# Performance work log

Measured on AMD Instinct MI355X. Metric: run time of the kernel, lower is better.

The kernel has to match this reference:

```python
import jax, jax.numpy as jnp
import numpy as np

N = 50000      # nodes
E = 600000     # edges
D = 128        # in_channels
H = 128        # hidden_channels
C = 16         # out_channels
L = 3          # num GIN layers
G = 512        # graphs in batch
BN_EPS = 1e-5


def setup_inputs() -> dict:
    key = jax.random.key(0)
    ks = jax.random.split(key, 18)
    s = 0.05
    x = jax.random.normal(ks[0], (N, D), jnp.float32)
    edge_index = jax.random.randint(ks[1], (2, E), 0, N, dtype=jnp.int32)
    batch = jnp.sort(jax.random.randint(ks[2], (N,), 0, G, dtype=jnp.int32))
    # per-layer GIN MLP params (in_channels == hidden, so layers stack uniformly)
    W1s = jax.random.normal(ks[3], (L, D, H), jnp.float32) * s
    b1s = jnp.zeros((L, H), jnp.float32)
    g1s = jnp.ones((L, H), jnp.float32)    # inner BatchNorm gamma
    be1s = jnp.zeros((L, H), jnp.float32)  # inner BatchNorm beta
    W2s = jax.random.normal(ks[4], (L, H, H), jnp.float32) * s
    b2s = jnp.zeros((L, H), jnp.float32)
    gns = jnp.ones((L, H), jnp.float32)    # outer (post-conv) BatchNorm gamma
    bns = jnp.zeros((L, H), jnp.float32)
    # classifier head
    Wc1 = jax.random.normal(ks[5], (H, H), jnp.float32) * s
    bc1 = jnp.zeros((H,), jnp.float32)
    gc = jnp.ones((H,), jnp.float32)
    bec = jnp.zeros((H,), jnp.float32)
    Wc2 = jax.random.normal(ks[6], (H, C), jnp.float32) * s
    bc2 = jnp.zeros((C,), jnp.float32)
    return dict(x=x, edge_index=edge_index, batch=batch, W1s=W1s, b1s=b1s,
                g1s=g1s, be1s=be1s, W2s=W2s, b2s=b2s, gns=gns, bns=bns,
                Wc1=Wc1, bc1=bc1, gc=gc, bec=bec, Wc2=Wc2, bc2=bc2)


def _bn(h, gamma, beta):
    # BatchNorm1d in training mode: batch statistics over the node/row dim
    m = jnp.mean(h, axis=0)
    v = jnp.mean((h - m) ** 2, axis=0)
    return gamma * (h - m) * jax.lax.rsqrt(v + BN_EPS) + beta


def reference(x, edge_index, batch, W1s, b1s, g1s, be1s, W2s, b2s, gns, bns,
              Wc1, bc1, gc, bec, Wc2, bc2):
    src, dst = edge_index[0], edge_index[1]
    h = x
    for l in range(L):
        # GINConv, eps=0: mlp((1+eps)*x_i + sum_{j->i} x_j)
        agg = jax.ops.segment_sum(h[src], dst, num_segments=N) + h
        z = agg @ W1s[l] + b1s[l]
        z = jax.nn.relu(_bn(z, g1s[l], be1s[l]))
        z = z @ W2s[l] + b2s[l]
        h = jax.nn.relu(_bn(z, gns[l], bns[l]))
    # global mean pool over graphs
    counts = jax.ops.segment_sum(jnp.ones((N,), h.dtype), batch, num_segments=G)
    pooled = jax.ops.segment_sum(h, batch, num_segments=G) / jnp.maximum(counts, 1.0)[:, None]
    z = pooled @ Wc1 + bc1
    z = jax.nn.relu(_bn(z, gc, bec))
    return z @ Wc2 + bc2  # [G, C]
```

## Files before the change

### kernel.cpp

```cpp
#include <hip/hip_runtime.h>
#include <hip/hip_fp16.h>

#define NN 50000
#define NE 600000
#define DIM 128
#define NG 512
#define OC 16
#define BN_EPS 1e-5f

typedef __attribute__((ext_vector_type(8))) short short8v;
typedef __attribute__((ext_vector_type(8))) _Float16 half8v;
typedef __attribute__((ext_vector_type(2))) _Float16 h2v;
typedef __attribute__((ext_vector_type(4))) float f32x4;

__device__ inline float hbits2f(short s) {
    __half_raw hr; hr.x = (unsigned short)s;
    return __half2float(__half(hr));
}
__device__ inline short f2hbits(float f) {
    __half h = __float2half(f);
    short r;
    __builtin_memcpy(&r, &h, 2);
    return r;
}
__device__ inline h2v u2p(unsigned u) {
    h2v h;
    __builtin_memcpy(&h, &u, 4);
    return h;
}
__device__ inline unsigned p2u(h2v h) {
    unsigned u;
    __builtin_memcpy(&u, &h, 4);
    return u;
}
__device__ inline h2v f2p(float a, float b) {
    h2v h;
    h[0] = (_Float16)a;
    h[1] = (_Float16)b;
    return h;
}

__global__ void k_setup(const float* __restrict__ W1s, const float* __restrict__ W2s,
                        const float* __restrict__ Wc1, unsigned short* __restrict__ wfrag,
                        const int* __restrict__ dstv, int* __restrict__ deg,
                        const float* __restrict__ x, __half* __restrict__ Ht) {
    int b = blockIdx.x;
    int t = threadIdx.x;
    if (b < 56) {
        int idx = b * 256 + t;
        int lane = idx & 63;
        int k0 = (idx >> 6) & 3;
        int ct = (idx >> 8) & 7;
        int m = idx >> 11;
        const float* Wsrc = (m < 3) ? (W1s + (size_t)m * 16384)
                          : (m < 6) ? (W2s + (size_t)(m - 3) * 16384)
                                    : Wc1;
        int colc = ct * 16 + (lane & 15);
        int kbase = k0 * 32 + (lane >> 4) * 8;
        short8v hi, lo;
#pragma unroll
        for (int j = 0; j < 8; j++) {
            float w = Wsrc[(size_t)(kbase + j) * 128 + colc];
            short hb = f2hbits(w);
            hi[j] = hb;
            lo[j] = f2hbits(w - hbits2f(hb));
        }
        size_t fo = ((size_t)(ct * 4 + k0) * 64 + lane) * 8;
        *(short8v*)(wfrag + (size_t)(m * 2 + 0) * 16384 + fo) = hi;
        *(short8v*)(wfrag + (size_t)(m * 2 + 1) * 16384 + fo) = lo;
    } else if (b < 2400) {
        int i = (b - 56) * 256 + t;
        if (i < NE) atomicAdd(&deg[dstv[i]], 1);
    } else {
        int i = (b - 2400) * 256 + t;
        float4 v = ((const float4*)x)[i];
        uint2 pk;
        pk.x = p2u(f2p(v.x, v.y));
        pk.y = p2u(f2p(v.z, v.w));
        ((uint2*)Ht)[i] = pk;
    }
}

__global__ void k_scan1(const int* __restrict__ deg, int* __restrict__ pre,
                        int* __restrict__ bsum, int n) {
    __shared__ int lds[1024];
    int t = threadIdx.x;
    int i = blockIdx.x * 1024 + t;
    int v = (i < n) ? deg[i] : 0;
    lds[t] = v;
    __syncthreads();
#pragma unroll
    for (int off = 1; off < 1024; off <<= 1) {
        int add = (t >= off) ? lds[t - off] : 0;
        __syncthreads();
        lds[t] += add;
        __syncthreads();
    }
    if (i < n) pre[i] = lds[t] - v;
    if (t == 1023) bsum[blockIdx.x] = lds[1023];
}

__global__ void k_scan3(const int* __restrict__ pre, const int* __restrict__ bsum,
                        const int* __restrict__ batch,
                        int* __restrict__ row_start, int* __restrict__ cursor,
                        int* __restrict__ gstart, int n, int nb) {
    __shared__ int boff[64];
    int t = threadIdx.x;
    if (t < 64) {
        int v = (t < nb) ? bsum[t] : 0;
        int orig = v;
#pragma unroll
        for (int off = 1; off < 64; off <<= 1) {
            int u = __shfl_up(v, off);
            if (t >= off) v += u;
        }
        boff[t] = v - orig;
    }
    __syncthreads();
    int i = blockIdx.x * blockDim.x + t;
    if (i < n) {
        int r = pre[i] + boff[i >> 10];
        row_start[i] = r;
        cursor[i] = r;
        int b = batch[i];
        int bp = (i == 0) ? -1 : batch[i - 1];
        for (int g = bp + 1; g <= b; g++) gstart[g] = i;
        if (i == n - 1) {
            for (int g = b + 1; g <= NG; g++) gstart[g] = n;
        }
    }
    if (i == 0) row_start[n] = NE;
}

__global__ void k_scatter(const int* __restrict__ src, const int* __restrict__ dst,
                          int* __restrict__ cursor, int* __restrict__ col, int e) {
    int i = blockIdx.x * blockDim.x + threadIdx.x;
    if (i < e) {
        int d = dst[i];
        int p = atomicAdd(&cursor[d], 1);
        col[p] = src[i];
    }
}

template <int TRANSFORM>
__global__ void k_aggregate_h(const __half* __restrict__ Ht, const int* __restrict__ rs,
                              const int* __restrict__ col,
                              const float* __restrict__ stats, const float* __restrict__ gamma,
                              const float* __restrict__ beta, float invn,
                              __half* __restrict__ out, int n) {
    __shared__ float sst[256];
    int tid = threadIdx.x;
    if (TRANSFORM && tid < 128) {
        float s = stats[tid], q = stats[128 + tid];
        float m = s * invn;
        float var = fmaxf(q * invn - m * m, 0.f);
        float r = rsqrtf(var + BN_EPS);
        float sc = gamma[tid] * r;
        sst[tid] = sc;
        sst[128 + tid] = beta[tid] - m * sc;
    }
    if (TRANSFORM) __syncthreads();

    int node = blockIdx.x * 8 + (tid >> 5);
    if (node >= n) return;
    int hl = tid & 31;
    int c = hl * 4;
    h2v sc2[2], sh2[2];
    if (TRANSFORM) {
        sc2[0] = f2p(sst[c], sst[c + 1]);
        sc2[1] = f2p(sst[c + 2], sst[c + 3]);
        sh2[0] = f2p(sst[128 + c], sst[129 + c]);
        sh2[1] = f2p(sst[130 + c], sst[131 + c]);
    }
    const h2v zero2 = f2p(0.f, 0.f);
    const uint2* Hp = (const uint2*)Ht;

#define TRF2(H, P) (TRANSFORM ? __builtin_elementwise_max((H) * sc2[P] + sh2[P], zero2) : (H))
    h2v a0, a1, b0, b1;
    {
        uint2 uv = Hp[(size_t)node * 32 + hl];
        a0 = TRF2(u2p(uv.x), 0);
        a1 = TRF2(u2p(uv.y), 1);
        b0 = zero2;
        b1 = zero2;
    }
    int s = rs[node], e = rs[node + 1];
    int i = s;
    for (; i + 3 < e; i += 4) {
        int j0 = col[i], j1 = col[i + 1], j2 = col[i + 2], j3 = col[i + 3];
        uint2 u0 = Hp[(size_t)j0 * 32 + hl];
        uint2 u1 = Hp[(size_t)j1 * 32 + hl];
        uint2 u2e = Hp[(size_t)j2 * 32 + hl];
        uint2 u3 = Hp[(size_t)j3 * 32 + hl];
        a0 += TRF2(u2p(u0.x), 0);
        a1 += TRF2(u2p(u0.y), 1);
        b0 += TRF2(u2p(u1.x), 0);
        b1 += TRF2(u2p(u1.y), 1);
        a0 += TRF2(u2p(u2e.x), 0);
        a1 += TRF2(u2p(u2e.y), 1);
        b0 += TRF2(u2p(u3.x), 0);
        b1 += TRF2(u2p(u3.y), 1);
    }
    for (; i < e; i++) {
        uint2 u0 = Hp[(size_t)col[i] * 32 + hl];
        b0 += TRF2(u2p(u0.x), 0);
        b1 += TRF2(u2p(u0.y), 1);
    }
#undef TRF2
    a0 += b0;
    a1 += b1;
    uint2 o;
    o.x = p2u(a0);
    o.y = p2u(a1);
    ((uint2*)out)[(size_t)node * 32 + hl] = o;
}

#define MFMA16(A8, B8, C4) __builtin_amdgcn_mfma_f32_16x16x32_f16(A8, B8, C4, 0, 0, 0)

#define STORE_STATS(ACT, ACC0, ACC1, SUB)                                          \
    if (ACT) {                                                                     \
        int rowb = (SUB) * 16 + kb * 4;                                            \
        _Pragma("unroll")                                                          \
        for (int j = 0; j < 4; j++) {                                              \
            size_t i0 = (size_t)(rowb + j) * 128 + ct0 * 16 + rlo;                 \
            size_t i1 = (size_t)(rowb + j) * 128 + ct1 * 16 + rlo;                 \
            if (ZHALF) {                                                           \
                ((__half*)Zout)[i0] = __float2half(ACC0[j]);                       \
                ((__half*)Zout)[i1] = __float2half(ACC1[j]);                       \
            } else {                                                               \
                ((float*)Zout)[i0] = ACC0[j];                                      \
                ((float*)Zout)[i1] = ACC1[j];                                      \
            }                                                                      \
        }                                                                          \
        float s0 = ACC0[0] + ACC0[1] + ACC0[2] + ACC0[3];                          \
        float q0 = ACC0[0]*ACC0[0] + ACC0[1]*ACC0[1] + ACC0[2]*ACC0[2] + ACC0[3]*ACC0[3]; \
        float s1 = ACC1[0] + ACC1[1] + ACC1[2] + ACC1[3];                          \
        float q1 = ACC1[0]*ACC1[0] + ACC1[1]*ACC1[1] + ACC1[2]*ACC1[2] + ACC1[3]*ACC1[3]; \
        s0 += __shfl_xor(s0, 16); s0 += __shfl_xor(s0, 32);                        \
        q0 += __shfl_xor(q0, 16); q0 += __shfl_xor(q0, 32);                        \
        s1 += __shfl_xor(s1, 16); s1 += __shfl_xor(s1, 32);                        \
        q1 += __shfl_xor(q1, 16); q1 += __shfl_xor(q1, 32);                        \
        if (kb == 0) {                                                             \
            atomicAdd(&sred[ct0 * 16 + rlo], s0);                                  \
            atomicAdd(&sred[128 + ct0 * 16 + rlo], q0);                            \
            atomicAdd(&sred[ct1 * 16 + rlo], s1);                                  \
            atomicAdd(&sred[128 + ct1 * 16 + rlo], q1);                            \
        }                                                                          \
    }

template <int TRANSFORM, int ZHALF>
__global__ __launch_bounds__(256) void k_gemm_mfma(
        const __half* __restrict__ A, const unsigned short* __restrict__ wfragm,
        const float* __restrict__ bias,
        const float* __restrict__ statsIn, const float* __restrict__ gamma,
        const float* __restrict__ beta, float invn,
        void* __restrict__ Zout, float* __restrict__ statsOut, int nsub) {
    __shared__ short8v wldsHi[1024];
    __shared__ short8v wldsLo[1024];
    __shared__ float sred[256];
    __shared__ unsigned ssth[128];
    int tid = threadIdx.x;
    int wid = tid >> 6, lane = tid & 63;
    int sub0 = (blockIdx.x * 4 + wid) * 2;
    bool act0 = sub0 < nsub, act1 = sub0 + 1 < nsub;
    int rlo = lane & 15, kb = lane >> 4;

    sred[tid] = 0.f;
    if (TRANSFORM && tid < 64) {
        int c0 = tid * 2;
        float s0 = statsIn[c0], q0 = statsIn[128 + c0];
        float m0 = s0 * invn;
        float r0 = rsqrtf(fmaxf(q0 * invn - m0 * m0, 0.f) + BN_EPS);
        float sca = gamma[c0] * r0;
        float sha = beta[c0] - m0 * sca;
        float s1 = statsIn[c0 + 1], q1 = statsIn[129 + c0];
        float m1 = s1 * invn;
        float r1 = rsqrtf(fmaxf(q1 * invn - m1 * m1, 0.f) + BN_EPS);
        float scb = gamma[c0 + 1] * r1;
        float shb = beta[c0 + 1] - m1 * scb;
        ssth[tid] = p2u(f2p(sca, scb));
        ssth[64 + tid] = p2u(f2p(sha, shb));
    }
    __syncthreads();

    const h2v zero2 = f2p(0.f, 0.f);
    half8v af[2][4];
#pragma unroll
    for (int ss = 0; ss < 2; ss++) {
        bool act = ss ? act1 : act0;
        if (act) {
            const uint4* ap = (const uint4*)(A + ((size_t)(sub0 + ss) * 16 + rlo) * 128);
#pragma unroll
            for (int k0 = 0; k0 < 4; k0++) {
                uint4 uv = ap[k0 * 4 + kb];
                if (TRANSFORM) {
                    int hc = (k0 * 32 + kb * 8) >> 1;
                    uv.x = p2u(__builtin_elementwise_max(
                        u2p(uv.x) * u2p(ssth[hc + 0]) + u2p(ssth[64 + hc + 0]), zero2));
                    uv.y = p2u(__builtin_elementwise_max(
                        u2p(uv.y) * u2p(ssth[hc + 1]) + u2p(ssth[64 + hc + 1]), zero2));
                    uv.z = p2u(__builtin_elementwise_max(
                        u2p(uv.z) * u2p(ssth[hc + 2]) + u2p(ssth[64 + hc + 2]), zero2));
                    uv.w = p2u(__builtin_elementwise_max(
                        u2p(uv.w) * u2p(ssth[hc + 3]) + u2p(ssth[64 + hc + 3]), zero2));
                }
                __builtin_memcpy(&af[ss][k0], &uv, 16);
            }
        } else {
#pragma unroll
            for (int k0 = 0; k0 < 4; k0++) af[ss][k0] = half8v{0,0,0,0,0,0,0,0};
        }
    }

    const float4* wsrc = (const float4*)wfragm;
    float4* dH = (float4*)wldsHi;
    float4* dL = (float4*)wldsLo;

#pragma unroll
    for (int p = 0; p < 2; p++) {
        if (p) __syncthreads();
#pragma unroll
        for (int i = 0; i < 4; i++) {
            dH[tid + 256 * i] = wsrc[p * 1024 + tid + 256 * i];
            dL[tid + 256 * i] = wsrc[2048 + p * 1024 + tid + 256 * i];
        }
        __syncthreads();
#pragma unroll
        for (int cc = 0; cc < 2; cc++) {
            int ctp = 2 * p + cc;
            int ct0 = ctp * 2, ct1 = ct0 + 1;
            int l0 = ct0 - 4 * p, l1 = ct1 - 4 * p;
            float bb0 = bias[ct0 * 16 + rlo], bb1 = bias[ct1 * 16 + rlo];
            f32x4 acc00 = {bb0, bb0, bb0, bb0};
            f32x4 acc01 = {bb1, bb1, bb1, bb1};
            f32x4 acc10 = {bb0, bb0, bb0, bb0};
            f32x4 acc11 = {bb1, bb1, bb1, bb1};
#pragma unroll
            for (int k0 = 0; k0 < 4; k0++) {
                half8v bh0, bh1, bl0, bl1;
                __builtin_memcpy(&bh0, &wldsHi[(l0 * 4 + k0) * 64 + lane], 16);
                __builtin_memcpy(&bh1, &wldsHi[(l1 * 4 + k0) * 64 + lane], 16);
                __builtin_memcpy(&bl0, &wldsLo[(l0 * 4 + k0) * 64 + lane], 16);
                __builtin_memcpy(&bl1, &wldsLo[(l1 * 4 + k0) * 64 + lane], 16);
                acc00 = MFMA16(af[0][k0], bh0, acc00);
                acc10 = MFMA16(af[1][k0], bh0, acc10);
                acc01 = MFMA16(af[0][k0], bh1, acc01);
                acc11 = MFMA16(af[1][k0], bh1, acc11);
                acc00 = MFMA16(af[0][k0], bl0, acc00);
                acc10 = MFMA16(af[1][k0], bl0, acc10);
                acc01 = MFMA16(af[0][k0], bl1, acc01);
                acc11 = MFMA16(af[1][k0], bl1, acc11);
            }
            STORE_STATS(act0, acc00, acc01, sub0);
            STORE_STATS(act1, acc10, acc11, sub0 + 1);
        }
    }
    __syncthreads();
    if (tid < 128) {
        atomicAdd(&statsOut[tid], sred[tid]);
        atomicAdd(&statsOut[128 + tid], sred[128 + tid]);
    }
}

__global__ void k_pool_seg(const __half* __restrict__ H, const int* __restrict__ gstart,
                           const float* __restrict__ stats, const float* __restrict__ gamma,
                           const float* __restrict__ beta, float invn,
                           __half* __restrict__ out) {
    int g = blockIdx.x;
    int s = gstart[g], e = gstart[g + 1];
    int t = threadIdx.x;
    int lane = t & 63, wave = t >> 6;
    int c0 = lane * 2;
    float sc0, sc1, sh0, sh1;
    {
        float s0 = stats[c0], q0 = stats[128 + c0];
        float m0 = s0 * invn;
        float r0 = rsqrtf(fmaxf(q0 * invn - m0 * m0, 0.f) + BN_EPS);
        sc0 = gamma[c0] * r0; sh0 = beta[c0] - m0 * sc0;
        float s1 = stats[c0 + 1], q1 = stats[129 + c0];
        float m1 = s1 * invn;
        float r1 = rsqrtf(fmaxf(q1 * invn - m1 * m1, 0.f) + BN_EPS);
        sc1 = gamma[c0 + 1] * r1; sh1 = beta[c0 + 1] - m1 * sc1;
    }
    const __half2* Hp = (const __half2*)H;
    float ax = 0.f, ay = 0.f;
    for (int r = s + wave; r < e; r += 4) {
        float2 v = __half22float2(Hp[(size_t)r * 64 + lane]);
        ax += fmaxf(fmaf(v.x, sc0, sh0), 0.f);
        ay += fmaxf(fmaf(v.y, sc1, sh1), 0.f);
    }
    __shared__ float red[2][256];
    red[0][t] = ax;
    red[1][t] = ay;
    __syncthreads();
    if (wave == 0) {
        float inv = 1.f / fmaxf((float)(e - s), 1.f);
        float sx = red[0][lane] + red[0][64 + lane] + red[0][128 + lane] + red[0][192 + lane];
        float sy = red[1][lane] + red[1][64 + lane] + red[1][128 + lane] + red[1][192 + lane];
        ((__half2*)out)[g * 64 + lane] = __floats2half2_rn(sx * inv, sy * inv);
    }
}

__global__ void k_final(const float* __restrict__ Zh, const float* __restrict__ stats,
                        const float* __restrict__ gamma, const float* __restrict__ beta,
                        float invn, const float* __restrict__ Wc2,
                        const float* __restrict__ bc2, float* __restrict__ out) {
    __shared__ float Wl[128 * 16];
    __shared__ float Al[32 * 128];
    int tid = threadIdx.x;
    int kc = tid & 127;
    float s = stats[kc], q = stats[128 + kc];
    float m = s * invn;
    float rs = rsqrtf(fmaxf(q * invn - m * m, 0.f) + BN_EPS);
    float sck = gamma[kc] * rs;
    float shk = beta[kc] - m * sck;
#pragma unroll
    for (int i = 0; i < 4; i++) Wl[tid + 512 * i] = Wc2[tid + 512 * i];
#pragma unroll
    for (int i = 0; i < 8; i++) {
        int idx = tid + 512 * i;
        int gl = idx >> 7, k = idx & 127;
        float a = Zh[(size_t)(blockIdx.x * 32 + gl) * 128 + k];
        Al[idx] = fmaxf(fmaf(a, sck, shk), 0.f);
    }
    __syncthreads();
    int g = tid >> 4, c = tid & 15;
    float acc = bc2[c];
#pragma unroll 8
    for (int k = 0; k < 128; k++) acc = fmaf(Al[g * 128 + k], Wl[k * 16 + c], acc);
    out[(size_t)(blockIdx.x * 32 + g) * 16 + c] = acc;
}

extern "C" void kernel_launch(void* const* d_in, const int* in_sizes, int n_in,
                              void* d_out, int out_size, void* d_ws, size_t ws_size,
                              hipStream_t stream) {
    (void)in_sizes; (void)n_in; (void)out_size; (void)ws_size;
    const float* x    = (const float*)d_in[0];
    const int*   ei   = (const int*)d_in[1];
    const int*   srcv = ei;
    const int*   dstv = ei + NE;
    const int*   batch = (const int*)d_in[2];
    const float* W1s = (const float*)d_in[3];
    const float* b1s = (const float*)d_in[4];
    const float* g1s = (const float*)d_in[5];
    const float* be1s = (const float*)d_in[6];
    const float* W2s = (const float*)d_in[7];
    const float* b2s = (const float*)d_in[8];
    const float* gns = (const float*)d_in[9];
    const float* bns = (const float*)d_in[10];
    const float* Wc1 = (const float*)d_in[11];
    const float* bc1 = (const float*)d_in[12];
    const float* gc  = (const float*)d_in[13];
    const float* bec = (const float*)d_in[14];
    const float* Wc2 = (const float*)d_in[15];
    const float* bc2 = (const float*)d_in[16];
    float* out = (float*)d_out;

    char* ws = (char*)d_ws;
    size_t off = 0;
    auto alloc = [&](size_t bytes) -> char* {
        char* p = ws + off;
        off += (bytes + 255) & ~(size_t)255;
        return p;
    };
    int*   deg     = (int*)alloc(50048 * 4);
    float* statsZ  = (float*)alloc(7 * 256 * 4);
    size_t zeroBytes = off;
    int*   row_start = (int*)alloc((NN + 64) * 4);
    int*   cursor    = (int*)alloc((NN + 64) * 4);
    int*   pre       = (int*)alloc((NN + 64) * 4);
    int*   bsum      = (int*)alloc(64 * 4);
    int*   col       = (int*)alloc((NE + 64) * 4);
    int*   gstart    = (int*)alloc((NG + 1) * 4);
    unsigned short* wfrag = (unsigned short*)alloc((size_t)7 * 2 * 16384 * 2);
    __half* Ht     = (__half*)alloc((size_t)NN * 128 * 2);
    __half* aggH   = (__half*)alloc((size_t)NN * 128 * 2);
    __half* bufBh  = (__half*)alloc((size_t)NN * 128 * 2);
    __half* bufCh  = (__half*)alloc((size_t)NN * 128 * 2);
    __half* headAh = (__half*)alloc((size_t)NG * 128 * 2);
    float*  bufF   = (float*)alloc((size_t)NG * 128 * 4);

    hipMemsetAsync(d_ws, 0, zeroBytes, stream);

    k_setup<<<8650, 256, 0, stream>>>(W1s, W2s, Wc1, wfrag, dstv, deg, x, Ht);

    int nb = (NN + 1023) / 1024;
    k_scan1<<<nb, 1024, 0, stream>>>(deg, pre, bsum, NN);
    k_scan3<<<(NN + 255) / 256, 256, 0, stream>>>(pre, bsum, batch, row_start, cursor,
                                                  gstart, NN, nb);
    k_scatter<<<(NE + 255) / 256, 256, 0, stream>>>(srcv, dstv, cursor, col, NE);

    int aggGrid = NN / 8;
    int nsub = NN / 16;
    int gGrid = (nsub + 7) / 8;
    float invN = 1.f / NN;

    for (int l = 0; l < 3; l++) {
        float* s1 = statsZ + (size_t)(2 * l) * 256;
        float* s2 = statsZ + (size_t)(2 * l + 1) * 256;
        if (l == 0)
            k_aggregate_h<0><<<aggGrid, 256, 0, stream>>>(
                Ht, row_start, col, nullptr, nullptr, nullptr, 0.f, aggH, NN);
        else
            k_aggregate_h<1><<<aggGrid, 256, 0, stream>>>(
                bufCh, row_start, col, statsZ + (size_t)(2 * l - 1) * 256,
                gns + (l - 1) * 128, bns + (l - 1) * 128, invN, aggH, NN);
        k_gemm_mfma<0, 1><<<gGrid, 256, 0, stream>>>(
            aggH, wfrag + (size_t)(2 * l) * 16384, b1s + l * 128,
            nullptr, nullptr, nullptr, 0.f, bufBh, s1, nsub);
        k_gemm_mfma<1, 1><<<gGrid, 256, 0, stream>>>(
            bufBh, wfrag + (size_t)(2 * (3 + l)) * 16384, b2s + l * 128,
            s1, g1s + l * 128, be1s + l * 128, invN, bufCh, s2, nsub);
    }

    float* s2last = statsZ + (size_t)5 * 256;
    float* sHead  = statsZ + (size_t)6 * 256;
    k_pool_seg<<<NG, 256, 0, stream>>>(bufCh, gstart, s2last, gns + 2 * 128,
                                       bns + 2 * 128, invN, headAh);
    k_gemm_mfma<0, 0><<<4, 256, 0, stream>>>(
        headAh, wfrag + (size_t)12 * 16384, bc1,
        nullptr, nullptr, nullptr, 0.f, bufF, sHead, NG / 16);
    k_final<<<16, 512, 0, stream>>>(bufF, sHead, gc, bec, 1.f / NG, Wc2, bc2, out);
}
```

Measured before the change: 309.0 us.

## Fuse neighbor aggregation into first GEMM with MFMA fragment-layout accumulation

Replaces the separate aggregation kernel and first MLP GEMM with one kernel. Each wave gathers neighbor rows for 16 nodes directly into registers laid out as MFMA A-fragments, then multiplies them by W1 from LDS and accumulates the BN statistics. This removes the write and re-read of the aggregated intermediate buffer and one launch per layer. In exchange, each lane now gathers irregular 16-byte chunks from four places per neighbor row, and the per-wave load is set by the degrees of 16 nodes, which can worsen load imbalance.

Result: slower. 330.0 us (+6.8%).

```diff
diff --git a/kernel.cpp b/kernel.cpp
--- a/kernel.cpp
+++ b/kernel.cpp
@@ -142,80 +142,169 @@
     }
 }
 
+#define MFMA16(A8, B8, C4) __builtin_amdgcn_mfma_f32_16x16x32_f16(A8, B8, C4, 0, 0, 0)
+
 template <int TRANSFORM>
-__global__ void k_aggregate_h(const __half* __restrict__ Ht, const int* __restrict__ rs,
-                              const int* __restrict__ col,
-                              const float* __restrict__ stats, const float* __restrict__ gamma,
-                              const float* __restrict__ beta, float invn,
-                              __half* __restrict__ out, int n) {
-    __shared__ float sst[256];
+__global__ __launch_bounds__(256) void k_gemm1g(
+        const __half* __restrict__ Ht, const int* __restrict__ rs,
+        const int* __restrict__ col,
+        const float* __restrict__ statsIn, const float* __restrict__ gamma,
+        const float* __restrict__ beta, float invn,
+        const unsigned short* __restrict__ wfragm, const float* __restrict__ bias,
+        __half* __restrict__ Zout, float* __restrict__ statsOut, int nsub) {
+    __shared__ short8v wldsHi[1024];
+    __shared__ short8v wldsLo[1024];
+    __shared__ float sred[256];
+    __shared__ unsigned ssth[128];
     int tid = threadIdx.x;
-    if (TRANSFORM && tid < 128) {
-        float s = stats[tid], q = stats[128 + tid];
-        float m = s * invn;
-        float var = fmaxf(q * invn - m * m, 0.f);
-        float r = rsqrtf(var + BN_EPS);
-        float sc = gamma[tid] * r;
-        sst[tid] = sc;
-        sst[128 + tid] = beta[tid] - m * sc;
-    }
-    if (TRANSFORM) __syncthreads();
-
-    int node = blockIdx.x * 8 + (tid >> 5);
-    if (node >= n) return;
-    int hl = tid & 31;
-    int c = hl * 4;
-    h2v sc2[2], sh2[2];
+    int wid = tid >> 6, lane = tid & 63;
+    int sub = blockIdx.x * 4 + wid;
+    bool act = sub < nsub;
+    int rlo = lane & 15, kb = lane >> 4;
+
+    sred[tid] = 0.f;
+    if (TRANSFORM && tid < 64) {
+        int c0 = tid * 2;
+        float s0 = statsIn[c0], q0 = statsIn[128 + c0];
+        float m0 = s0 * invn;
+        float r0 = rsqrtf(fmaxf(q0 * invn - m0 * m0, 0.f) + BN_EPS);
+        float sca = gamma[c0] * r0;
+        float sha = beta[c0] - m0 * sca;
+        float s1 = statsIn[c0 + 1], q1 = statsIn[129 + c0];
+        float m1 = s1 * invn;
+        float r1 = rsqrtf(fmaxf(q1 * invn - m1 * m1, 0.f) + BN_EPS);
+        float scb = gamma[c0 + 1] * r1;
+        float shb = beta[c0 + 1] - m1 * scb;
+        ssth[tid] = p2u(f2p(sca, scb));
+        ssth[64 + tid] = p2u(f2p(sha, shb));
+    }
+    __syncthreads();
+
+    const h2v zero2 = f2p(0.f, 0.f);
+    h2v sc2[16], sh2[16];
     if (TRANSFORM) {
-        sc2[0] = f2p(sst[c], sst[c + 1]);
-        sc2[1] = f2p(sst[c + 2], sst[c + 3]);
-        sh2[0] = f2p(sst[128 + c], sst[129 + c]);
-        sh2[1] = f2p(sst[130 + c], sst[131 + c]);
-    }
-    const h2v zero2 = f2p(0.f, 0.f);
-    const uint2* Hp = (const uint2*)Ht;
-
-#define TRF2(H, P) (TRANSFORM ? __builtin_elementwise_max((H) * sc2[P] + sh2[P], zero2) : (H))
-    h2v a0, a1, b0, b1;
-    {
-        uint2 uv = Hp[(size_t)node * 32 + hl];
-        a0 = TRF2(u2p(uv.x), 0);
-        a1 = TRF2(u2p(uv.y), 1);
-        b0 = zero2;
-        b1 = zero2;
-    }
-    int s = rs[node], e = rs[node + 1];
-    int i = s;
-    for (; i + 3 < e; i += 4) {
-        int j0 = col[i], j1 = col[i + 1], j2 = col[i + 2], j3 = col[i + 3];
-        uint2 u0 = Hp[(size_t)j0 * 32 + hl];
-        uint2 u1 = Hp[(size_t)j1 * 32 + hl];
-        uint2 u2e = Hp[(size_t)j2 * 32 + hl];
-        uint2 u3 = Hp[(size_t)j3 * 32 + hl];
-        a0 += TRF2(u2p(u0.x), 0);
-        a1 += TRF2(u2p(u0.y), 1);
-        b0 += TRF2(u2p(u1.x), 0);
-        b1 += TRF2(u2p(u1.y), 1);
-        a0 += TRF2(u2p(u2e.x), 0);
-        a1 += TRF2(u2p(u2e.y), 1);
-        b0 += TRF2(u2p(u3.x), 0);
-        b1 += TRF2(u2p(u3.y), 1);
-    }
-    for (; i < e; i++) {
-        uint2 u0 = Hp[(size_t)col[i] * 32 + hl];
-        b0 += TRF2(u2p(u0.x), 0);
-        b1 += TRF2(u2p(u0.y), 1);
-    }
-#undef TRF2
-    a0 += b0;
-    a1 += b1;
-    uint2 o;
-    o.x = p2u(a0);
-    o.y = p2u(a1);
-    ((uint2*)out)[(size_t)node * 32 + hl] = o;
-}
-
-#define MFMA16(A8, B8, C4) __builtin_amdgcn_mfma_f32_16x16x32_f16(A8, B8, C4, 0, 0, 0)
+#pragma unroll
+        for (int k0 = 0; k0 < 4; k0++) {
+            int hc = (k0 * 32 + kb * 8) >> 1;
+#pragma unroll
+            for (int p = 0; p < 4; p++) {
+                sc2[k0 * 4 + p] = u2p(ssth[hc + p]);
+                sh2[k0 * 4 + p] = u2p(ssth[64 + hc + p]);
+            }
+        }
+    }
+
+#define TRFG(H, I) (TRANSFORM ? __builtin_elementwise_max((H) * sc2[I] + sh2[I], zero2) : (H))
+#define ACC4(UV, K0)                                                   \
+    acc[(K0) * 4 + 0] += TRFG(u2p((UV).x), (K0) * 4 + 0);              \
+    acc[(K0) * 4 + 1] += TRFG(u2p((UV).y), (K0) * 4 + 1);              \
+    acc[(K0) * 4 + 2] += TRFG(u2p((UV).z), (K0) * 4 + 2);              \
+    acc[(K0) * 4 + 3] += TRFG(u2p((UV).w), (K0) * 4 + 3);
+
+    h2v acc[16];
+#pragma unroll
+    for (int j = 0; j < 16; j++) acc[j] = zero2;
+
+    const uint4* Hp = (const uint4*)Ht;
+    if (act) {
+        int node = sub * 16 + rlo;
+        {
+            uint4 u0 = Hp[(size_t)node * 16 + 0 + kb];
+            uint4 u1 = Hp[(size_t)node * 16 + 4 + kb];
+            uint4 u2 = Hp[(size_t)node * 16 + 8 + kb];
+            uint4 u3 = Hp[(size_t)node * 16 + 12 + kb];
+            ACC4(u0, 0) ACC4(u1, 1) ACC4(u2, 2) ACC4(u3, 3)
+        }
+        int s = rs[node], e = rs[node + 1];
+        int i = s;
+        for (; i + 1 < e; i += 2) {
+            size_t b0 = (size_t)col[i] * 16;
+            size_t b1 = (size_t)col[i + 1] * 16;
+            uint4 a0 = Hp[b0 + kb],      a1 = Hp[b0 + 4 + kb];
+            uint4 a2 = Hp[b0 + 8 + kb],  a3 = Hp[b0 + 12 + kb];
+            uint4 c0 = Hp[b1 + kb],      c1 = Hp[b1 + 4 + kb];
+            uint4 c2 = Hp[b1 + 8 + kb],  c3 = Hp[b1 + 12 + kb];
+            ACC4(a0, 0) ACC4(a1, 1) ACC4(a2, 2) ACC4(a3, 3)
+            ACC4(c0, 0) ACC4(c1, 1) ACC4(c2, 2) ACC4(c3, 3)
+        }
+        if (i < e) {
+            size_t b0 = (size_t)col[i] * 16;
+            uint4 a0 = Hp[b0 + kb],      a1 = Hp[b0 + 4 + kb];
+            uint4 a2 = Hp[b0 + 8 + kb],  a3 = Hp[b0 + 12 + kb];
+            ACC4(a0, 0) ACC4(a1, 1) ACC4(a2, 2) ACC4(a3, 3)
+        }
+    }
+#undef ACC4
+#undef TRFG
+
+    half8v af[4];
+#pragma unroll
+    for (int k0 = 0; k0 < 4; k0++) __builtin_memcpy(&af[k0], &acc[k0 * 4], 16);
+
+    const float4* wsrc = (const float4*)wfragm;
+    float4* dH = (float4*)wldsHi;
+    float4* dL = (float4*)wldsLo;
+
+#pragma unroll
+    for (int p = 0; p < 2; p++) {
+        if (p) __syncthreads();
+#pragma unroll
+        for (int i = 0; i < 4; i++) {
+            dH[tid + 256 * i] = wsrc[p * 1024 + tid + 256 * i];
+            dL[tid + 256 * i] = wsrc[2048 + p * 1024 + tid + 256 * i];
+        }
+        __syncthreads();
+#pragma unroll
+        for (int cc = 0; cc < 2; cc++) {
+            int ctp = 2 * p + cc;
+            int ct0 = ctp * 2, ct1 = ct0 + 1;
+            int l0 = ct0 - 4 * p, l1 = ct1 - 4 * p;
+            float bb0 = bias[ct0 * 16 + rlo], bb1 = bias[ct1 * 16 + rlo];
+            f32x4 acc0 = {bb0, bb0, bb0, bb0};
+            f32x4 acc1 = {bb1, bb1, bb1, bb1};
+#pragma unroll
+            for (int k0 = 0; k0 < 4; k0++) {
+                half8v bh0, bh1, bl0, bl1;
+                __builtin_memcpy(&bh0, &wldsHi[(l0 * 4 + k0) * 64 + lane], 16);
+                __builtin_memcpy(&bh1, &wldsHi[(l1 * 4 + k0) * 64 + lane], 16);
+                __builtin_memcpy(&bl0, &wldsLo[(l0 * 4 + k0) * 64 + lane], 16);
+                __builtin_memcpy(&bl1, &wldsLo[(l1 * 4 + k0) * 64 + lane], 16);
+                acc0 = MFMA16(af[k0], bh0, acc0);
+                acc1 = MFMA16(af[k0], bh1, acc1);
+                acc0 = MFMA16(af[k0], bl0, acc0);
+                acc1 = MFMA16(af[k0], bl1, acc1);
+            }
+            if (act) {
+#pragma unroll
+                for (int j = 0; j < 4; j++) {
+                    size_t i0 = (size_t)(sub * 16 + kb * 4 + j) * 128 + ct0 * 16 + rlo;
+                    size_t i1 = (size_t)(sub * 16 + kb * 4 + j) * 128 + ct1 * 16 + rlo;
+                    Zout[i0] = __float2half(acc0[j]);
+                    Zout[i1] = __float2half(acc1[j]);
+                }
+                float s0 = acc0[0] + acc0[1] + acc0[2] + acc0[3];
+                float q0 = acc0[0]*acc0[0] + acc0[1]*acc0[1] + acc0[2]*acc0[2] + acc0[3]*acc0[3];
+                float s1 = acc1[0] + acc1[1] + acc1[2] + acc1[3];
+                float q1 = acc1[0]*acc1[0] + acc1[1]*acc1[1] + acc1[2]*acc1[2] + acc1[3]*acc1[3];
+                s0 += __shfl_xor(s0, 16); s0 += __shfl_xor(s0, 32);
+                q0 += __shfl_xor(q0, 16); q0 += __shfl_xor(q0, 32);
+                s1 += __shfl_xor(s1, 16); s1 += __shfl_xor(s1, 32);
+                q1 += __shfl_xor(q1, 16); q1 += __shfl_xor(q1, 32);
+                if (kb == 0) {
+                    atomicAdd(&sred[ct0 * 16 + rlo], s0);
+                    atomicAdd(&sred[128 + ct0 * 16 + rlo], q0);
+                    atomicAdd(&sred[ct1 * 16 + rlo], s1);
+                    atomicAdd(&sred[128 + ct1 * 16 + rlo], q1);
+                }
+            }
+        }
+    }
+    __syncthreads();
+    if (tid < 128) {
+        atomicAdd(&statsOut[tid], sred[tid]);
+        atomicAdd(&statsOut[128 + tid], sred[128 + tid]);
+    }
+}
 
 #define STORE_STATS(ACT, ACC0, ACC1, SUB)                                          \
     if (ACT) {                                                                     \
@@ -474,7 +563,6 @@
     int*   gstart    = (int*)alloc((NG + 1) * 4);
     unsigned short* wfrag = (unsigned short*)alloc((size_t)7 * 2 * 16384 * 2);
     __half* Ht     = (__half*)alloc((size_t)NN * 128 * 2);
-    __half* aggH   = (__half*)alloc((size_t)NN * 128 * 2);
     __half* bufBh  = (__half*)alloc((size_t)NN * 128 * 2);
     __half* bufCh  = (__half*)alloc((size_t)NN * 128 * 2);
     __half* headAh = (__half*)alloc((size_t)NG * 128 * 2);
@@ -490,8 +578,8 @@
                                                   gstart, NN, nb);
     k_scatter<<<(NE + 255) / 256, 256, 0, stream>>>(srcv, dstv, cursor, col, NE);
 
-    int aggGrid = NN / 8;
     int nsub = NN / 16;
+    int g1Grid = (nsub + 3) / 4;
     int gGrid = (nsub + 7) / 8;
     float invN = 1.f / NN;
 
@@ -499,15 +587,14 @@
         float* s1 = statsZ + (size_t)(2 * l) * 256;
         float* s2 = statsZ + (size_t)(2 * l + 1) * 256;
         if (l == 0)
-            k_aggregate_h<0><<<aggGrid, 256, 0, stream>>>(
-                Ht, row_start, col, nullptr, nullptr, nullptr, 0.f, aggH, NN);
+            k_gemm1g<0><<<g1Grid, 256, 0, stream>>>(
+                Ht, row_start, col, nullptr, nullptr, nullptr, 0.f,
+                wfrag + (size_t)(2 * l) * 16384, b1s + l * 128, bufBh, s1, nsub);
         else
-            k_aggregate_h<1><<<aggGrid, 256, 0, stream>>>(
+            k_gemm1g<1><<<g1Grid, 256, 0, stream>>>(
                 bufCh, row_start, col, statsZ + (size_t)(2 * l - 1) * 256,
-                gns + (l - 1) * 128, bns + (l - 1) * 128, invN, aggH, NN);
-        k_gemm_mfma<0, 1><<<gGrid, 256, 0, stream>>>(
-            aggH, wfrag + (size_t)(2 * l) * 16384, b1s + l * 128,
-            nullptr, nullptr, nullptr, 0.f, bufBh, s1, nsub);
+                gns + (l - 1) * 128, bns + (l - 1) * 128, invN,
+                wfrag + (size_t)(2 * l) * 16384, b1s + l * 128, bufBh, s1, nsub);
         k_gemm_mfma<1, 1><<<gGrid, 256, 0, stream>>>(
             bufBh, wfrag + (size_t)(2 * (3 + l)) * 16384, b2s + l * 128,
             s1, g1s + l * 128, be1s + l * 128, invN, bufCh, s2, nsub);
```

## Fuse classifier head GEMM, BN stats and final linear into one-block kernel

Applied to the files above, without the earlier changes.

Replaces the head GEMM kernel (4 blocks) and the final BN+linear kernel (16 blocks) with a single 512-thread single-block kernel. It computes the MFMA head GEMM, reduces the BN statistics in shared memory, then applies BN/ReLU and the output projection. This drops one launch and the global stats round trip, at the cost of running all head work on one CU. It also adds launch bounds with occupancy 6 to the aggregation kernel.

New measurement: 372.6 us. 1.21x slower.

```diff
diff --git a/kernel.cpp b/kernel.cpp
--- a/kernel.cpp
+++ b/kernel.cpp
@@ -143,11 +143,12 @@
 }
 
 template <int TRANSFORM>
-__global__ void k_aggregate_h(const __half* __restrict__ Ht, const int* __restrict__ rs,
-                              const int* __restrict__ col,
-                              const float* __restrict__ stats, const float* __restrict__ gamma,
-                              const float* __restrict__ beta, float invn,
-                              __half* __restrict__ out, int n) {
+__global__ __launch_bounds__(256, 6) void k_aggregate_h(
+        const __half* __restrict__ Ht, const int* __restrict__ rs,
+        const int* __restrict__ col,
+        const float* __restrict__ stats, const float* __restrict__ gamma,
+        const float* __restrict__ beta, float invn,
+        __half* __restrict__ out, int n) {
     __shared__ float sst[256];
     int tid = threadIdx.x;
     if (TRANSFORM && tid < 128) {
@@ -401,34 +402,92 @@
     }
 }
 
-__global__ void k_final(const float* __restrict__ Zh, const float* __restrict__ stats,
-                        const float* __restrict__ gamma, const float* __restrict__ beta,
-                        float invn, const float* __restrict__ Wc2,
-                        const float* __restrict__ bc2, float* __restrict__ out) {
-    __shared__ float Wl[128 * 16];
+__global__ __launch_bounds__(512) void k_headfinal(
+        const __half* __restrict__ headAh, const unsigned short* __restrict__ wfragW,
+        const float* __restrict__ bc1, const float* __restrict__ gc,
+        const float* __restrict__ bec, const float* __restrict__ Wc2,
+        const float* __restrict__ bc2, float* __restrict__ bufF,
+        float* __restrict__ out) {
+    __shared__ short8v wH[2048];
+    __shared__ short8v wL[2048];
+    __shared__ float sred[256];
+    __shared__ float wc2l[128 * 16];
+    __shared__ float scl[128], shl[128];
     __shared__ float Al[32 * 128];
     int tid = threadIdx.x;
-    int kc = tid & 127;
-    float s = stats[kc], q = stats[128 + kc];
-    float m = s * invn;
-    float rs = rsqrtf(fmaxf(q * invn - m * m, 0.f) + BN_EPS);
-    float sck = gamma[kc] * rs;
-    float shk = beta[kc] - m * sck;
-#pragma unroll
-    for (int i = 0; i < 4; i++) Wl[tid + 512 * i] = Wc2[tid + 512 * i];
-#pragma unroll
-    for (int i = 0; i < 8; i++) {
-        int idx = tid + 512 * i;
-        int gl = idx >> 7, k = idx & 127;
-        float a = Zh[(size_t)(blockIdx.x * 32 + gl) * 128 + k];
-        Al[idx] = fmaxf(fmaf(a, sck, shk), 0.f);
-    }
-    __syncthreads();
+    if (tid < 256) sred[tid] = 0.f;
+    const float4* wsrc = (const float4*)wfragW;
+    float4* dH = (float4*)wH;
+    float4* dL = (float4*)wL;
+#pragma unroll
+    for (int i = 0; i < 4; i++) {
+        dH[tid + 512 * i] = wsrc[tid + 512 * i];
+        dL[tid + 512 * i] = wsrc[2048 + tid + 512 * i];
+    }
+#pragma unroll
+    for (int i = 0; i < 4; i++) wc2l[tid + 512 * i] = Wc2[tid + 512 * i];
+    __syncthreads();
+
+    int wid = tid >> 6, lane = tid & 63;
+    int rlo = lane & 15, kb = lane >> 4;
+    for (int sub = wid; sub < NG / 16; sub += 8) {
+        half8v af[4];
+        const uint4* ap = (const uint4*)(headAh + ((size_t)sub * 16 + rlo) * 128);
+#pragma unroll
+        for (int k0 = 0; k0 < 4; k0++) {
+            uint4 uv = ap[k0 * 4 + kb];
+            __builtin_memcpy(&af[k0], &uv, 16);
+        }
+#pragma unroll
+        for (int ct = 0; ct < 8; ct++) {
+            float bb = bc1[ct * 16 + rlo];
+            f32x4 acc = {bb, bb, bb, bb};
+#pragma unroll
+            for (int k0 = 0; k0 < 4; k0++) {
+                half8v bh, bl;
+                __builtin_memcpy(&bh, &wH[(ct * 4 + k0) * 64 + lane], 16);
+                __builtin_memcpy(&bl, &wL[(ct * 4 + k0) * 64 + lane], 16);
+                acc = MFMA16(af[k0], bh, acc);
+                acc = MFMA16(af[k0], bl, acc);
+            }
+#pragma unroll
+            for (int j = 0; j < 4; j++)
+                bufF[(size_t)(sub * 16 + kb * 4 + j) * 128 + ct * 16 + rlo] = acc[j];
+            float s0 = acc[0] + acc[1] + acc[2] + acc[3];
+            float q0 = acc[0]*acc[0] + acc[1]*acc[1] + acc[2]*acc[2] + acc[3]*acc[3];
+            s0 += __shfl_xor(s0, 16); s0 += __shfl_xor(s0, 32);
+            q0 += __shfl_xor(q0, 16); q0 += __shfl_xor(q0, 32);
+            if (kb == 0) {
+                atomicAdd(&sred[ct * 16 + rlo], s0);
+                atomicAdd(&sred[128 + ct * 16 + rlo], q0);
+            }
+        }
+    }
+    __syncthreads();
+    if (tid < 128) {
+        float s = sred[tid], q = sred[128 + tid];
+        float m = s * (1.f / NG);
+        float rs = rsqrtf(fmaxf(q * (1.f / NG) - m * m, 0.f) + BN_EPS);
+        float sc = gc[tid] * rs;
+        scl[tid] = sc;
+        shl[tid] = bec[tid] - m * sc;
+    }
     int g = tid >> 4, c = tid & 15;
-    float acc = bc2[c];
+    for (int it = 0; it < 16; it++) {
+        __syncthreads();
+#pragma unroll
+        for (int i = 0; i < 8; i++) {
+            int idx = tid + 512 * i;
+            int gl = idx >> 7, k = idx & 127;
+            float a = bufF[(size_t)(it * 32 + gl) * 128 + k];
+            Al[idx] = fmaxf(fmaf(a, scl[k], shl[k]), 0.f);
+        }
+        __syncthreads();
+        float accO = bc2[c];
 #pragma unroll 8
-    for (int k = 0; k < 128; k++) acc = fmaf(Al[g * 128 + k], Wl[k * 16 + c], acc);
-    out[(size_t)(blockIdx.x * 32 + g) * 16 + c] = acc;
+        for (int k = 0; k < 128; k++) accO = fmaf(Al[g * 128 + k], wc2l[k * 16 + c], accO);
+        out[(size_t)(it * 32 + g) * 16 + c] = accO;
+    }
 }
 
 extern "C" void kernel_launch(void* const* d_in, const int* in_sizes, int n_in,
@@ -514,11 +573,8 @@
     }
 
     float* s2last = statsZ + (size_t)5 * 256;
-    float* sHead  = statsZ + (size_t)6 * 256;
     k_pool_seg<<<NG, 256, 0, stream>>>(bufCh, gstart, s2last, gns + 2 * 128,
                                        bns + 2 * 128, invN, headAh);
-    k_gemm_mfma<0, 0><<<4, 256, 0, stream>>>(
-        headAh, wfrag + (size_t)12 * 16384, bc1,
-        nullptr, nullptr, nullptr, 0.f, bufF, sHead, NG / 16);
-    k_final<<<16, 512, 0, stream>>>(bufF, sHead, gc, bec, 1.f / NG, Wc2, bc2, out);
-}
+    k_headfinal<<<1, 512, 0, stream>>>(headAh, wfrag + (size_t)12 * 16384,
+                                       bc1, gc, bec, Wc2, bc2, bufF, out);
+}
```
